# Kernel optimization log

Hardware: AMD Instinct MI355X
Metric: run time of the kernel (lower is better)

## Reference

```python
import jax, jax.numpy as jnp
import numpy as np

D_MODEL = 1024
N_HEADS = 16
CHUNK = 64
EPS = 1e-6


def elu_plus_1(x):
    return jax.nn.elu(x) + 1.0


def setup_inputs() -> dict:
    key = jax.random.key(0)
    kx, kq, kk, kv, ko = jax.random.split(key, 5)
    B, T = 4, 4096
    # xavier_uniform for square (D, D) weights: limit = sqrt(6/(D+D))
    lim = float(np.sqrt(6.0 / (D_MODEL + D_MODEL)))
    mk = lambda k: jax.random.uniform(k, (D_MODEL, D_MODEL), jnp.float32, -lim, lim)
    return {
        "x": jax.random.normal(kx, (B, T, D_MODEL), jnp.float32),
        "W_q": mk(kq),
        "W_k": mk(kk),
        "W_v": mk(kv),
        "W_o": mk(ko),
    }


def reference(x, W_q, W_k, W_v, W_o):
    B, T, D = x.shape
    H = N_HEADS
    dk = D // H
    dv = dk
    C = CHUNK
    N = T // C  # T chosen divisible by chunk size (no padding needed)

    q = (x @ W_q.T).reshape(B, T, H, dk)
    k = (x @ W_k.T).reshape(B, T, H, dk)
    v = (x @ W_v.T).reshape(B, T, H, dv)

    phi_q = elu_plus_1(q).reshape(B, N, C, H, dk)
    phi_k = elu_plus_1(k).reshape(B, N, C, H, dk)
    vc = v.reshape(B, N, C, H, dv)

    # Per-chunk key-value outer products and key sums, then exclusive prefix
    # sums over chunks give the carried state S and normalizer z at each
    # chunk's start (same math as the sequential chunk loop).
    KV = jnp.einsum('bnchk,bnchv->bnhkv', phi_k, vc)      # (B,N,H,dk,dv)
    Ksum = phi_k.sum(axis=2)                               # (B,N,C->sum,H,dk) -> (B,N,H,dk)
    KV_cum = jnp.cumsum(KV, axis=1)
    Ksum_cum = jnp.cumsum(Ksum, axis=1)
    S_prefix = jnp.concatenate([jnp.zeros_like(KV_cum[:, :1]), KV_cum[:, :-1]], axis=1)
    z_prefix = jnp.concatenate([jnp.zeros_like(Ksum_cum[:, :1]), Ksum_cum[:, :-1]], axis=1)

    # Inter-chunk contribution from carried state
    inter = jnp.einsum('bnchk,bnhkv->bnchv', phi_q, S_prefix)   # (B,N,C,H,dv)
    z_inter = jnp.einsum('bnchk,bnhk->bnch', phi_q, z_prefix)   # (B,N,C,H)

    # Intra-chunk causal attention
    mask = jnp.tril(jnp.ones((C, C), dtype=x.dtype))
    attn = jnp.einsum('bnihk,bnjhk->bnhij', phi_q, phi_k) * mask  # (B,N,H,C,C)
    intra = jnp.einsum('bnhij,bnjhv->bnihv', attn, vc)            # (B,N,C,H,dv)
    z_intra = attn.sum(axis=-1).transpose(0, 1, 3, 2)             # (B,N,C,H)

    denom = jnp.clip((z_inter + z_intra)[..., None], 1e-6, None)
    y = (inter + intra) / denom                                   # (B,N,C,H,dv)
    y = y.reshape(B, T, H * dv)
    return y @ W_o.T
```

## Files before the change

kernel.cpp:

```cpp
#include <hip/hip_runtime.h>


typedef unsigned short u16;
typedef float  f32x4 __attribute__((ext_vector_type(4)));
typedef short  b16x8 __attribute__((ext_vector_type(8)));
typedef u16    u16x4 __attribute__((ext_vector_type(4)));
typedef u16    u16x8 __attribute__((ext_vector_type(8)));

#define DEVINL __device__ __forceinline__

DEVINL u16 f2b(float f) {
  unsigned u = __float_as_uint(f);
  return (u16)((u + 0x7fffu + ((u >> 16) & 1u)) >> 16);
}
DEVINL float b2f(u16 s) { return __uint_as_float(((unsigned)s) << 16); }

DEVINL f32x4 mfma16(b16x8 a, b16x8 b, f32x4 c) {
  return __builtin_amdgcn_mfma_f32_16x16x32_bf16(a, b, c, 0, 0, 0);
}

DEVINL float phi_elu1(float v) { return v > 0.f ? v + 1.f : __expf(v); }

__global__ void cvt_all(const float* __restrict__ x,
                        const float* __restrict__ Wq, const float* __restrict__ Wk,
                        const float* __restrict__ Wv, const float* __restrict__ Wo,
                        u16* __restrict__ xb, u16* __restrict__ wqb,
                        u16* __restrict__ wkb, u16* __restrict__ wvb,
                        u16* __restrict__ wob) {
  const float* in;
  u16* out;
  int blk0, nblk, n8;
  const int b = blockIdx.x;
  if (b < 2048) {
    in = x; out = xb; blk0 = b; nblk = 2048; n8 = 2097152;
  } else {
    const int w = (b - 2048) >> 7;
    blk0 = (b - 2048) & 127; nblk = 128; n8 = 131072;
    switch (w) {
      case 0: in = Wq; out = wqb; break;
      case 1: in = Wk; out = wkb; break;
      case 2: in = Wv; out = wvb; break;
      default: in = Wo; out = wob; break;
    }
  }
  const int stride = nblk * 256;
  for (int i = blk0 * 256 + threadIdx.x; i < n8; i += stride) {
    const float* p = in + (size_t)i * 8;
    f32x4 a = *(const f32x4*)p;
    f32x4 c = *(const f32x4*)(p + 4);
    u16x8 o;
    o[0] = f2b(a[0]); o[1] = f2b(a[1]); o[2] = f2b(a[2]); o[3] = f2b(a[3]);
    o[4] = f2b(c[0]); o[5] = f2b(c[1]); o[6] = f2b(c[2]); o[7] = f2b(c[3]);
    *(u16x8*)(out + (size_t)i * 8) = o;
  }
}

#define BAR_SB()                                                                \
  do {                                                                          \
    __builtin_amdgcn_s_barrier();                                               \
    __builtin_amdgcn_sched_barrier(0);                                          \
  } while (0)

#define GLOAD(s_, d_)                                                           \
  __builtin_amdgcn_global_load_lds(                                             \
      (const __attribute__((address_space(1))) void*)(s_),                      \
      (__attribute__((address_space(3))) void*)(d_), 16, 0, 0)

template <bool PHI, typename OT>
__global__ __launch_bounds__(512, 2) void gemm256g(const u16* __restrict__ A,
                                                   const u16* __restrict__ B,
                                                   OT* __restrict__ C, int M, int N) {
  __shared__ char lds[131072];
  const int tid = threadIdx.x, wid = tid >> 6, l = tid & 63;
  const int l15 = l & 15, lg = l >> 4;
  const int wr = wid >> 2, wc = wid & 3;
  const int ntn = N >> 8;
  const int nwg = gridDim.x, bid = blockIdx.x;
  const int cpx = nwg >> 3;
  const int sb = (bid & 7) * cpx + (bid >> 3);
  const int tm = sb / ntn, tn = sb - tm * ntn;
  const int colX0 = (lg * 16) ^ ((l15 & 7) << 4);
  const int colX1 = (64 + lg * 16) ^ ((l15 & 7) << 4);
  char* ldsA = lds + wr * 16384 + l15 * 128;
  char* ldsB = lds + 32768 + (wc >> 1) * 16384 + ((wc & 1) * 64 + l15) * 128;
  const int srow = tid >> 3;
  const int scol = ((((tid & 7) * 16) ^ ((srow & 7) << 4)) >> 1);
  const u16* sA = A + (size_t)(tm * 256 + srow) * 1024 + scol;
  const u16* sB = B + (size_t)(tn * 256 + srow) * 1024 + scol;
  char* ldsStage = lds + wid * 1024;

#define STAGE(tt, h)                                                            \
  do {                                                                          \
    const u16* s_ = ((h) < 2 ? sA : sB) + (size_t)(((h) & 1) * 128) * 1024 +    \
                    (size_t)(tt) * 64;                                          \
    char* d_ = ldsStage + (((tt) & 1) << 16) + ((h) < 2 ? 0 : 32768) +          \
               (((h) & 1) << 14);                                               \
    GLOAD(s_, d_);                                                              \
    GLOAD(s_ + 64 * 1024, d_ + 8192);                                           \
  } while (0)

  f32x4 acc[8][4];
#pragma unroll
  for (int i = 0; i < 8; i++)
#pragma unroll
    for (int j = 0; j < 4; j++) acc[i][j] = f32x4{0.f, 0.f, 0.f, 0.f};

  STAGE(0, 0); STAGE(0, 1); STAGE(0, 2); STAGE(0, 3);
  STAGE(1, 2); STAGE(1, 3);
  asm volatile("s_waitcnt vmcnt(4)" ::: "memory");

  b16x8 a0[4], a1[4], b0[4], b1[4];
  for (int t = 0; t < 16; ++t) {
    const int cb = (t & 1) << 16;
    BAR_SB();
#pragma unroll
    for (int fm = 0; fm < 4; fm++) {
      a0[fm] = *(const b16x8*)(ldsA + cb + fm * 2048 + colX0);
      a1[fm] = *(const b16x8*)(ldsA + cb + (4 + fm) * 2048 + colX0);
    }
#pragma unroll
    for (int fn = 0; fn < 4; fn++) b0[fn] = *(const b16x8*)(ldsB + cb + fn * 2048 + colX0);
    if (t < 15) { STAGE(t + 1, 0); STAGE(t + 1, 1); }
    __builtin_amdgcn_s_setprio(1);
#pragma unroll
    for (int fm = 0; fm < 4; fm++)
#pragma unroll
      for (int fn = 0; fn < 4; fn++) {
        acc[fm][fn] = mfma16(a0[fm], b0[fn], acc[fm][fn]);
        acc[4 + fm][fn] = mfma16(a1[fm], b0[fn], acc[4 + fm][fn]);
      }
    __builtin_amdgcn_s_setprio(0);
    BAR_SB();
#pragma unroll
    for (int fm = 0; fm < 4; fm++) {
      a0[fm] = *(const b16x8*)(ldsA + cb + fm * 2048 + colX1);
      a1[fm] = *(const b16x8*)(ldsA + cb + (4 + fm) * 2048 + colX1);
    }
#pragma unroll
    for (int fn = 0; fn < 4; fn++) b1[fn] = *(const b16x8*)(ldsB + cb + fn * 2048 + colX1);
    if (t < 14) { STAGE(t + 2, 2); STAGE(t + 2, 3); }
    __builtin_amdgcn_s_setprio(1);
#pragma unroll
    for (int fm = 0; fm < 4; fm++)
#pragma unroll
      for (int fn = 0; fn < 4; fn++) {
        acc[fm][fn] = mfma16(a0[fm], b1[fn], acc[fm][fn]);
        acc[4 + fm][fn] = mfma16(a1[fm], b1[fn], acc[4 + fm][fn]);
      }
    __builtin_amdgcn_s_setprio(0);
    if (t < 14) asm volatile("s_waitcnt vmcnt(4)" ::: "memory");
    else        asm volatile("s_waitcnt vmcnt(0)" ::: "memory");
  }
#undef STAGE

#pragma unroll
  for (int fm = 0; fm < 8; ++fm)
#pragma unroll
    for (int fn = 0; fn < 4; ++fn)
#pragma unroll
      for (int r = 0; r < 4; ++r) {
        size_t grow = (size_t)tm * 256 + wr * 128 + fm * 16 + lg * 4 + r;
        size_t gcol = (size_t)tn * 256 + wc * 64 + fn * 16 + l15;
        float v = acc[fm][fn][r];
        if (PHI) v = phi_elu1(v);
        OT* p = C + grow * (size_t)N + gcol;
        if constexpr (sizeof(OT) == 2) *p = (OT)f2b(v);
        else                           *p = (OT)v;
      }
}

template <bool PHI, typename OT>
__global__ __launch_bounds__(256, 2) void gemm128(const u16* __restrict__ A,
                                                  const u16* __restrict__ B,
                                                  OT* __restrict__ C, int M, int N) {
  __shared__ char lds[65536];
  const int tid = threadIdx.x, wid = tid >> 6, l = tid & 63;
  const int l15 = l & 15, lg = l >> 4;
  const int wr = wid >> 1, wc = wid & 1;
  const int ntn = N >> 7;
  const int nwg = gridDim.x, bid = blockIdx.x;
  const int cpx = nwg >> 3;
  const int sb = (bid & 7) * cpx + (bid >> 3);
  const int tm = sb / ntn, tn = sb - tm * ntn;
  const int colX0 = (lg * 16) ^ ((l15 & 7) << 4);
  const int colX1 = (64 + lg * 16) ^ ((l15 & 7) << 4);
  char* ldsA = lds + (wr * 64 + l15) * 128;
  char* ldsB = lds + 16384 + (wc * 64 + l15) * 128;
  const int srow = tid >> 3;
  const int scol = ((((tid & 7) * 16) ^ ((srow & 7) << 4)) >> 1);
  const u16* sA = A + (size_t)(tm * 128 + srow) * 1024 + scol;
  const u16* sB = B + (size_t)(tn * 128 + srow) * 1024 + scol;
  char* ldsStage = lds + wid * 1024;

#define STAGE(tt, h)                                                            \
  do {                                                                          \
    const u16* s_ = ((h) < 2 ? sA : sB) + (size_t)(((h) & 1) * 64) * 1024 +     \
                    (size_t)(tt) * 64;                                          \
    char* d_ = ldsStage + (((tt) & 1) << 15) + ((h) < 2 ? 0 : 16384) +          \
               (((h) & 1) << 13);                                               \
    GLOAD(s_, d_);                                                              \
    GLOAD(s_ + 32 * 1024, d_ + 4096);                                           \
  } while (0)

  f32x4 acc[4][4];
#pragma unroll
  for (int i = 0; i < 4; i++)
#pragma unroll
    for (int j = 0; j < 4; j++) acc[i][j] = f32x4{0.f, 0.f, 0.f, 0.f};

  STAGE(0, 0); STAGE(0, 1); STAGE(0, 2); STAGE(0, 3);
  STAGE(1, 2); STAGE(1, 3);
  asm volatile("s_waitcnt vmcnt(4)" ::: "memory");

  b16x8 af[4], bf[4];
  for (int t = 0; t < 16; ++t) {
    const int cb = (t & 1) << 15;
    BAR_SB();
#pragma unroll
    for (int fm = 0; fm < 4; fm++) af[fm] = *(const b16x8*)(ldsA + cb + fm * 2048 + colX0);
#pragma unroll
    for (int fn = 0; fn < 4; fn++) bf[fn] = *(const b16x8*)(ldsB + cb + fn * 2048 + colX0);
    if (t < 15) { STAGE(t + 1, 0); STAGE(t + 1, 1); }
    __builtin_amdgcn_s_setprio(1);
#pragma unroll
    for (int fm = 0; fm < 4; fm++)
#pragma unroll
      for (int fn = 0; fn < 4; fn++) acc[fm][fn] = mfma16(af[fm], bf[fn], acc[fm][fn]);
    __builtin_amdgcn_s_setprio(0);
    BAR_SB();
#pragma unroll
    for (int fm = 0; fm < 4; fm++) af[fm] = *(const b16x8*)(ldsA + cb + fm * 2048 + colX1);
#pragma unroll
    for (int fn = 0; fn < 4; fn++) bf[fn] = *(const b16x8*)(ldsB + cb + fn * 2048 + colX1);
    if (t < 14) { STAGE(t + 2, 2); STAGE(t + 2, 3); }
    __builtin_amdgcn_s_setprio(1);
#pragma unroll
    for (int fm = 0; fm < 4; fm++)
#pragma unroll
      for (int fn = 0; fn < 4; fn++) acc[fm][fn] = mfma16(af[fm], bf[fn], acc[fm][fn]);
    __builtin_amdgcn_s_setprio(0);
    if (t < 14) asm volatile("s_waitcnt vmcnt(4)" ::: "memory");
    else        asm volatile("s_waitcnt vmcnt(0)" ::: "memory");
  }
#undef STAGE

#pragma unroll
  for (int fm = 0; fm < 4; ++fm)
#pragma unroll
    for (int fn = 0; fn < 4; ++fn)
#pragma unroll
      for (int r = 0; r < 4; ++r) {
        size_t grow = (size_t)tm * 128 + wr * 64 + fm * 16 + lg * 4 + r;
        size_t gcol = (size_t)tn * 128 + wc * 64 + fn * 16 + l15;
        float v = acc[fm][fn][r];
        if (PHI) v = phi_elu1(v);
        OT* p = C + grow * (size_t)N + gcol;
        if constexpr (sizeof(OT) == 2) *p = (OT)f2b(v);
        else                           *p = (OT)v;
      }
}

__global__ __launch_bounds__(256, 2) void kv_kernel(const u16* __restrict__ phiK,
                                                    const u16* __restrict__ vT,
                                                    u16* __restrict__ KVT,
                                                    float* __restrict__ Ksum) {
  __shared__ u16 tile[4][64][68];
  const int tid = threadIdx.x, wid = tid >> 6, l = tid & 63, l15 = l & 15, lg = l >> 4;
  const int bid = blockIdx.x, hg = bid & 3, bn = bid >> 2, n = bn & 63, b = bn >> 6;
  const int h = hg * 4 + wid;
  const size_t row0 = (size_t)b * 4096 + n * 64;
  const int dcol = h * 64;
  const size_t cb = (size_t)b * 4096 + n * 64 + lg * 8;

  b16x8 af[4][2];
#pragma unroll
  for (int fm = 0; fm < 4; fm++)
#pragma unroll
    for (int ks = 0; ks < 2; ks++)
      af[fm][ks] = *(const b16x8*)(vT + (size_t)(h * 64 + fm * 16 + l15) * 16384 + cb + ks * 32);

  u16 (*tw)[68] = tile[wid];
#pragma unroll
  for (int i = 0; i < 8; i++) {
    int tok = i * 8 + (l >> 3);
    int c8 = (l & 7) * 8;
    u16x8 v = *(const u16x8*)(phiK + (row0 + tok) * 1024 + dcol + c8);
    *(u16x4*)(&tw[tok][c8]) = u16x4{v[0], v[1], v[2], v[3]};
    *(u16x4*)(&tw[tok][c8 + 4]) = u16x4{v[4], v[5], v[6], v[7]};
  }
  __syncthreads();

  b16x8 bf[4][2];
#pragma unroll
  for (int fn = 0; fn < 4; fn++)
#pragma unroll
    for (int ks = 0; ks < 2; ks++) {
      b16x8 t;
#pragma unroll
      for (int j = 0; j < 8; j++)
        t[j] = (short)tw[lg * 8 + ks * 32 + j][fn * 16 + l15];
      bf[fn][ks] = t;
    }

  f32x4 acc[4][4];
#pragma unroll
  for (int i = 0; i < 4; i++)
#pragma unroll
    for (int j = 0; j < 4; j++) acc[i][j] = f32x4{0.f, 0.f, 0.f, 0.f};
#pragma unroll
  for (int ks = 0; ks < 2; ks++)
#pragma unroll
    for (int fm = 0; fm < 4; fm++)
#pragma unroll
      for (int fn = 0; fn < 4; fn++) acc[fm][fn] = mfma16(af[fm][ks], bf[fn][ks], acc[fm][fn]);

  float ksum[4] = {0.f, 0.f, 0.f, 0.f};
#pragma unroll
  for (int fn = 0; fn < 4; fn++) {
#pragma unroll
    for (int ks = 0; ks < 2; ks++)
#pragma unroll
      for (int j = 0; j < 8; j++) ksum[fn] += b2f((u16)bf[fn][ks][j]);
    ksum[fn] += __shfl_xor(ksum[fn], 16);
    ksum[fn] += __shfl_xor(ksum[fn], 32);
  }
  const size_t ob = (size_t)(b * 16 + h) * 64 + n;
  if (l < 16) {
#pragma unroll
    for (int fn = 0; fn < 4; fn++) Ksum[ob * 64 + fn * 16 + l15] = ksum[fn];
  }
#pragma unroll
  for (int fm = 0; fm < 4; fm++)
#pragma unroll
    for (int fn = 0; fn < 4; fn++)
#pragma unroll
      for (int r = 0; r < 4; r++)
        KVT[ob * 4096 + (size_t)(fm * 16 + lg * 4 + r) * 64 + fn * 16 + l15] =
            f2b(acc[fm][fn][r]);
}

__global__ __launch_bounds__(256) void scan_s(const u16* __restrict__ KVT,
                                              u16* __restrict__ ST,
                                              const float* __restrict__ Ksum,
                                              float* __restrict__ zpre) {
  if (blockIdx.x >= 512) {
    const int gi = (blockIdx.x - 512) * 256 + threadIdx.x;
    const size_t bh = gi >> 6;
    const int dk = gi & 63;
    float acc = 0.f;
    for (int n = 0; n < 64; n++) {
      size_t idx = (bh * 64 + n) * 64 + dk;
      zpre[idx] = acc;
      acc += Ksum[idx];
    }
    return;
  }
  const size_t base2 = (size_t)(blockIdx.x >> 3) * 64 * 2048 +
                       (blockIdx.x & 7) * 256 + threadIdx.x;
  const unsigned* KV32 = (const unsigned*)KVT;
  unsigned* ST32 = (unsigned*)ST;
  float ac0 = 0.f, ac1 = 0.f;
  unsigned v[4], w[4];
#pragma unroll
  for (int i = 0; i < 4; i++) v[i] = KV32[base2 + (size_t)i * 2048];
  for (int n = 0; n < 64; n += 4) {
    if (n < 60) {
#pragma unroll
      for (int i = 0; i < 4; i++) w[i] = KV32[base2 + (size_t)(n + 4 + i) * 2048];
    } else {
#pragma unroll
      for (int i = 0; i < 4; i++) w[i] = 0u;
    }
#pragma unroll
    for (int i = 0; i < 4; i++) {
      ST32[base2 + (size_t)(n + i) * 2048] =
          (unsigned)f2b(ac0) | ((unsigned)f2b(ac1) << 16);
      ac0 += b2f((u16)(v[i] & 0xffff));
      ac1 += b2f((u16)(v[i] >> 16));
    }
#pragma unroll
    for (int i = 0; i < 4; i++) v[i] = w[i];
  }
}

__global__ __launch_bounds__(256, 2) void attn_out(const u16* __restrict__ phiQ,
                                                   const u16* __restrict__ phiK,
                                                   const u16* __restrict__ vT,
                                                   const u16* __restrict__ ST,
                                                   const float* __restrict__ zpre,
                                                   u16* __restrict__ Y) {
  __shared__ char lds[4 * 8192 + 4 * 256];
  const int tid = threadIdx.x, wid = tid >> 6, l = tid & 63, l15 = l & 15, lg = l >> 4;
  const int bid = blockIdx.x, hg = bid & 3, bn = bid >> 2, n = bn & 63, b = bn >> 6;
  const int h = hg * 4 + wid;
  const size_t row0 = (size_t)b * 4096 + n * 64;
  const int dcol = h * 64;

  b16x8 qf[4][2];
#pragma unroll
  for (int fi = 0; fi < 4; fi++)
#pragma unroll
    for (int ks = 0; ks < 2; ks++)
      qf[fi][ks] = *(const b16x8*)(phiQ + (row0 + fi * 16 + l15) * 1024 + dcol + lg * 8 + ks * 32);

  f32x4 accT[4][4];
#pragma unroll
  for (int i = 0; i < 4; i++)
#pragma unroll
    for (int j = 0; j < 4; j++) accT[i][j] = f32x4{0.f, 0.f, 0.f, 0.f};
  {
    b16x8 kf[4][2];
#pragma unroll
    for (int fj = 0; fj < 4; fj++)
#pragma unroll
      for (int ks = 0; ks < 2; ks++)
        kf[fj][ks] = *(const b16x8*)(phiK + (row0 + fj * 16 + l15) * 1024 + dcol + lg * 8 + ks * 32);
#pragma unroll
    for (int ks = 0; ks < 2; ks++)
#pragma unroll
      for (int fj = 0; fj < 4; fj++)
#pragma unroll
        for (int fi = 0; fi < 4; fi++)
          accT[fj][fi] = mfma16(kf[fj][ks], qf[fi][ks], accT[fj][fi]);
  }

  const size_t zb = ((size_t)(b * 16 + h) * 64 + n) * 64;
  float zi[4] = {0.f, 0.f, 0.f, 0.f};
#pragma unroll
  for (int ks = 0; ks < 2; ks++) {
    f32x4 z0 = *(const f32x4*)(zpre + zb + lg * 8 + ks * 32);
    f32x4 z1 = *(const f32x4*)(zpre + zb + lg * 8 + ks * 32 + 4);
#pragma unroll
    for (int fi = 0; fi < 4; fi++)
#pragma unroll
      for (int j = 0; j < 4; j++) {
        zi[fi] += b2f((u16)qf[fi][ks][j])     * z0[j];
        zi[fi] += b2f((u16)qf[fi][ks][j + 4]) * z1[j];
      }
  }

  char* abuf = lds + wid * 8192;
  float zt[4] = {0.f, 0.f, 0.f, 0.f};
#pragma unroll
  for (int fi = 0; fi < 4; fi++) {
    const int i = fi * 16 + l15;
    const int swz = (i & 7) << 4;
#pragma unroll
    for (int fj = 0; fj < 4; fj++) {
      f32x4 v = accT[fj][fi];
#pragma unroll
      for (int r = 0; r < 4; r++) {
        int j = fj * 16 + lg * 4 + r;
        if (j > i) v[r] = 0.f;
        zt[fi] += v[r];
      }
      unsigned w0 = (unsigned)f2b(v[0]) | ((unsigned)f2b(v[1]) << 16);
      unsigned w1 = (unsigned)f2b(v[2]) | ((unsigned)f2b(v[3]) << 16);
      int jb = (fj * 16 + lg * 4) * 2;
      *(unsigned*)(abuf + i * 128 + (jb ^ swz)) = w0;
      *(unsigned*)(abuf + i * 128 + ((jb + 4) ^ swz)) = w1;
    }
  }

  float* dbuf = (float*)(lds + 32768 + wid * 256);
#pragma unroll
  for (int fi = 0; fi < 4; fi++) {
    float z = zi[fi] + zt[fi];
    z += __shfl_xor(z, 16);
    z += __shfl_xor(z, 32);
    float rd = 1.f / fmaxf(z, 1e-6f);
    if (l < 16) dbuf[fi * 16 + l15] = rd;
  }
  __syncthreads();

  b16x8 stf[4][2], vf[4][2];
  const size_t stb = ((size_t)(b * 16 + h) * 64 + n) * 4096;
#pragma unroll
  for (int fn = 0; fn < 4; fn++)
#pragma unroll
    for (int ks = 0; ks < 2; ks++) {
      stf[fn][ks] = *(const b16x8*)(ST + stb + (size_t)(fn * 16 + l15) * 64 + lg * 8 + ks * 32);
      vf[fn][ks]  = *(const b16x8*)(vT + (size_t)(dcol + fn * 16 + l15) * 16384 +
                                    (size_t)b * 4096 + n * 64 + lg * 8 + ks * 32);
    }
  f32x4 acc[4][4];
#pragma unroll
  for (int i = 0; i < 4; i++)
#pragma unroll
    for (int j = 0; j < 4; j++) acc[i][j] = f32x4{0.f, 0.f, 0.f, 0.f};
#pragma unroll
  for (int ks = 0; ks < 2; ks++)
#pragma unroll
    for (int fm = 0; fm < 4; fm++)
#pragma unroll
      for (int fn = 0; fn < 4; fn++) acc[fm][fn] = mfma16(qf[fm][ks], stf[fn][ks], acc[fm][fn]);
#pragma unroll
  for (int fm = 0; fm < 4; fm++) {
    const int i = fm * 16 + l15;
    const int swz = (i & 7) << 4;
#pragma unroll
    for (int ks = 0; ks < 2; ks++) {
      b16x8 af = *(const b16x8*)(abuf + i * 128 + ((ks * 64 + lg * 16) ^ swz));
#pragma unroll
      for (int fn = 0; fn < 4; fn++) acc[fm][fn] = mfma16(af, vf[fn][ks], acc[fm][fn]);
    }
  }

#pragma unroll
  for (int fm = 0; fm < 4; fm++)
#pragma unroll
    for (int r = 0; r < 4; r++) {
      float rd = dbuf[fm * 16 + lg * 4 + r];
#pragma unroll
      for (int fn = 0; fn < 4; fn++)
        Y[(row0 + fm * 16 + lg * 4 + r) * 1024 + dcol + fn * 16 + l15] =
            f2b(acc[fm][fn][r] * rd);
    }
}

extern "C" void kernel_launch(void* const* d_in, const int* in_sizes, int n_in,
                              void* d_out, int out_size, void* d_ws, size_t ws_size,
                              hipStream_t stream) {
  const float* x  = (const float*)d_in[0];
  const float* Wq = (const float*)d_in[1];
  const float* Wk = (const float*)d_in[2];
  const float* Wv = (const float*)d_in[3];
  const float* Wo = (const float*)d_in[4];
  float* out = (float*)d_out;

  char* ws = (char*)d_ws;
  size_t off = 0;
  auto alloc = [&](size_t bytes) -> char* {
    char* p = ws + off;
    off += (bytes + 255) & ~(size_t)255;
    return p;
  };
  u16*   xb   = (u16*)alloc(33554432);
  u16*   wqb  = (u16*)alloc(2097152);
  u16*   wkb  = (u16*)alloc(2097152);
  u16*   wvb  = (u16*)alloc(2097152);
  u16*   wob  = (u16*)alloc(2097152);
  u16*   phiQ = (u16*)alloc(33554432);
  u16*   phiK = (u16*)alloc(33554432);
  u16*   vT   = (u16*)alloc(33554432);
  u16*   KVT  = (u16*)alloc(33554432);
  float* Ksum = (float*)alloc(1048576);
  u16*   ST   = (u16*)alloc(33554432);
  float* zpre = (float*)alloc(1048576);
  u16*   y    = xb;

  cvt_all<<<2560, 256, 0, stream>>>(x, Wq, Wk, Wv, Wo, xb, wqb, wkb, wvb, wob);

  gemm128<true, u16><<<1024, 256, 0, stream>>>(xb, wqb, phiQ, 16384, 1024);
  gemm256g<true, u16><<<256, 512, 0, stream>>>(xb, wkb, phiK, 16384, 1024);
  gemm256g<false, u16><<<256, 512, 0, stream>>>(wvb, xb, vT, 1024, 16384);

  kv_kernel<<<1024, 256, 0, stream>>>(phiK, vT, KVT, Ksum);
  scan_s<<<528, 256, 0, stream>>>(KVT, ST, Ksum, zpre);
  attn_out<<<1024, 256, 0, stream>>>(phiQ, phiK, vT, ST, zpre, y);

  gemm256g<false, float><<<256, 512, 0, stream>>>(y, wob, out, 16384, 1024);
}
```

Measured before the change: 229.5 us.

## Replace Q-projection 128-tile GEMM with 256-tile GEMM loading B directly to registers

The Q projection GEMM changes from 128x128 tiles with 4 waves to 256x256 tiles with 8 waves. Only the A operand is staged through LDS. Each wave loads its B fragments straight from global memory into registers, double-buffered across K halves, with one barrier per K step instead of two. This is meant to raise data reuse and cut LDS traffic and synchronisation, at the cost of more registers and uncoalesced direct global loads for B.

```diff
diff --git a/kernel.cpp b/kernel.cpp
--- a/kernel.cpp
+++ b/kernel.cpp
@@ -170,88 +170,110 @@
 }
 
 template <bool PHI, typename OT>
-__global__ __launch_bounds__(256, 2) void gemm128(const u16* __restrict__ A,
-                                                  const u16* __restrict__ B,
-                                                  OT* __restrict__ C, int M, int N) {
+__global__ __launch_bounds__(512, 2) void gemm256d(const u16* __restrict__ A,
+                                                   const u16* __restrict__ B,
+                                                   OT* __restrict__ C, int M, int N) {
   __shared__ char lds[65536];
   const int tid = threadIdx.x, wid = tid >> 6, l = tid & 63;
   const int l15 = l & 15, lg = l >> 4;
-  const int wr = wid >> 1, wc = wid & 1;
-  const int ntn = N >> 7;
+  const int wr = wid >> 2, wc = wid & 3;
+  const int ntn = N >> 8;
   const int nwg = gridDim.x, bid = blockIdx.x;
   const int cpx = nwg >> 3;
   const int sb = (bid & 7) * cpx + (bid >> 3);
   const int tm = sb / ntn, tn = sb - tm * ntn;
   const int colX0 = (lg * 16) ^ ((l15 & 7) << 4);
   const int colX1 = (64 + lg * 16) ^ ((l15 & 7) << 4);
-  char* ldsA = lds + (wr * 64 + l15) * 128;
-  char* ldsB = lds + 16384 + (wc * 64 + l15) * 128;
+  char* ldsA = lds + wr * 16384 + l15 * 128;
   const int srow = tid >> 3;
   const int scol = ((((tid & 7) * 16) ^ ((srow & 7) << 4)) >> 1);
-  const u16* sA = A + (size_t)(tm * 128 + srow) * 1024 + scol;
-  const u16* sB = B + (size_t)(tn * 128 + srow) * 1024 + scol;
+  const u16* sA = A + (size_t)(tm * 256 + srow) * 1024 + scol;
   char* ldsStage = lds + wid * 1024;
-
-#define STAGE(tt, h)                                                            \
+  const u16* bp[4];
+#pragma unroll
+  for (int fn = 0; fn < 4; fn++)
+    bp[fn] = B + (size_t)(tn * 256 + wc * 64 + fn * 16 + l15) * 1024 + lg * 8;
+
+#define STAGEA(tt)                                                              \
   do {                                                                          \
-    const u16* s_ = ((h) < 2 ? sA : sB) + (size_t)(((h) & 1) * 64) * 1024 +     \
-                    (size_t)(tt) * 64;                                          \
-    char* d_ = ldsStage + (((tt) & 1) << 15) + ((h) < 2 ? 0 : 16384) +          \
-               (((h) & 1) << 13);                                               \
+    const u16* s_ = sA + (size_t)(tt) * 64;                                     \
+    char* d_ = ldsStage + (((tt) & 1) << 15);                                   \
     GLOAD(s_, d_);                                                              \
-    GLOAD(s_ + 32 * 1024, d_ + 4096);                                           \
+    GLOAD(s_ + 65536, d_ + 8192);                                               \
+    GLOAD(s_ + 131072, d_ + 16384);                                             \
+    GLOAD(s_ + 196608, d_ + 24576);                                             \
   } while (0)
 
-  f32x4 acc[4][4];
-#pragma unroll
-  for (int i = 0; i < 4; i++)
+  f32x4 acc[8][4];
+#pragma unroll
+  for (int i = 0; i < 8; i++)
 #pragma unroll
     for (int j = 0; j < 4; j++) acc[i][j] = f32x4{0.f, 0.f, 0.f, 0.f};
 
-  STAGE(0, 0); STAGE(0, 1); STAGE(0, 2); STAGE(0, 3);
-  STAGE(1, 2); STAGE(1, 3);
-  asm volatile("s_waitcnt vmcnt(4)" ::: "memory");
-
-  b16x8 af[4], bf[4];
+  b16x8 bk0[4], bk1[4];
+  STAGEA(0);
+#pragma unroll
+  for (int fn = 0; fn < 4; fn++) bk0[fn] = *(const b16x8*)(bp[fn]);
+#pragma unroll
+  for (int fn = 0; fn < 4; fn++) bk1[fn] = *(const b16x8*)(bp[fn] + 32);
+  asm volatile("s_waitcnt vmcnt(8)" ::: "memory");
+  BAR_SB();
+
+  b16x8 a0[4], a1[4];
   for (int t = 0; t < 16; ++t) {
     const int cb = (t & 1) << 15;
+#pragma unroll
+    for (int fm = 0; fm < 4; fm++) {
+      a0[fm] = *(const b16x8*)(ldsA + cb + fm * 2048 + colX0);
+      a1[fm] = *(const b16x8*)(ldsA + cb + (4 + fm) * 2048 + colX0);
+    }
+    if (t < 15) STAGEA(t + 1);
+    __builtin_amdgcn_s_setprio(1);
+#pragma unroll
+    for (int fm = 0; fm < 4; fm++)
+#pragma unroll
+      for (int fn = 0; fn < 4; fn++) {
+        acc[fm][fn] = mfma16(a0[fm], bk0[fn], acc[fm][fn]);
+        acc[4 + fm][fn] = mfma16(a1[fm], bk0[fn], acc[4 + fm][fn]);
+      }
+    __builtin_amdgcn_s_setprio(0);
+    if (t < 15) {
+#pragma unroll
+      for (int fn = 0; fn < 4; fn++) bk0[fn] = *(const b16x8*)(bp[fn] + (t + 1) * 64);
+    }
+#pragma unroll
+    for (int fm = 0; fm < 4; fm++) {
+      a0[fm] = *(const b16x8*)(ldsA + cb + fm * 2048 + colX1);
+      a1[fm] = *(const b16x8*)(ldsA + cb + (4 + fm) * 2048 + colX1);
+    }
+    __builtin_amdgcn_s_setprio(1);
+#pragma unroll
+    for (int fm = 0; fm < 4; fm++)
+#pragma unroll
+      for (int fn = 0; fn < 4; fn++) {
+        acc[fm][fn] = mfma16(a0[fm], bk1[fn], acc[fm][fn]);
+        acc[4 + fm][fn] = mfma16(a1[fm], bk1[fn], acc[4 + fm][fn]);
+      }
+    __builtin_amdgcn_s_setprio(0);
+    if (t < 15) {
+#pragma unroll
+      for (int fn = 0; fn < 4; fn++) bk1[fn] = *(const b16x8*)(bp[fn] + (t + 1) * 64 + 32);
+      asm volatile("s_waitcnt vmcnt(8)" ::: "memory");
+    } else {
+      asm volatile("s_waitcnt vmcnt(0)" ::: "memory");
+    }
     BAR_SB();
-#pragma unroll
-    for (int fm = 0; fm < 4; fm++) af[fm] = *(const b16x8*)(ldsA + cb + fm * 2048 + colX0);
-#pragma unroll
-    for (int fn = 0; fn < 4; fn++) bf[fn] = *(const b16x8*)(ldsB + cb + fn * 2048 + colX0);
-    if (t < 15) { STAGE(t + 1, 0); STAGE(t + 1, 1); }
-    __builtin_amdgcn_s_setprio(1);
-#pragma unroll
-    for (int fm = 0; fm < 4; fm++)
-#pragma unroll
-      for (int fn = 0; fn < 4; fn++) acc[fm][fn] = mfma16(af[fm], bf[fn], acc[fm][fn]);
-    __builtin_amdgcn_s_setprio(0);
-    BAR_SB();
-#pragma unroll
-    for (int fm = 0; fm < 4; fm++) af[fm] = *(const b16x8*)(ldsA + cb + fm * 2048 + colX1);
-#pragma unroll
-    for (int fn = 0; fn < 4; fn++) bf[fn] = *(const b16x8*)(ldsB + cb + fn * 2048 + colX1);
-    if (t < 14) { STAGE(t + 2, 2); STAGE(t + 2, 3); }
-    __builtin_amdgcn_s_setprio(1);
-#pragma unroll
-    for (int fm = 0; fm < 4; fm++)
-#pragma unroll
-      for (int fn = 0; fn < 4; fn++) acc[fm][fn] = mfma16(af[fm], bf[fn], acc[fm][fn]);
-    __builtin_amdgcn_s_setprio(0);
-    if (t < 14) asm volatile("s_waitcnt vmcnt(4)" ::: "memory");
-    else        asm volatile("s_waitcnt vmcnt(0)" ::: "memory");
-  }
-#undef STAGE
-
-#pragma unroll
-  for (int fm = 0; fm < 4; ++fm)
+  }
+#undef STAGEA
+
+#pragma unroll
+  for (int fm = 0; fm < 8; ++fm)
 #pragma unroll
     for (int fn = 0; fn < 4; ++fn)
 #pragma unroll
       for (int r = 0; r < 4; ++r) {
-        size_t grow = (size_t)tm * 128 + wr * 64 + fm * 16 + lg * 4 + r;
-        size_t gcol = (size_t)tn * 128 + wc * 64 + fn * 16 + l15;
+        size_t grow = (size_t)tm * 256 + wr * 128 + fm * 16 + lg * 4 + r;
+        size_t gcol = (size_t)tn * 256 + wc * 64 + fn * 16 + l15;
         float v = acc[fm][fn][r];
         if (PHI) v = phi_elu1(v);
         OT* p = C + grow * (size_t)N + gcol;
@@ -551,7 +573,7 @@
 
   cvt_all<<<2560, 256, 0, stream>>>(x, Wq, Wk, Wv, Wo, xb, wqb, wkb, wvb, wob);
 
-  gemm128<true, u16><<<1024, 256, 0, stream>>>(xb, wqb, phiQ, 16384, 1024);
+  gemm256d<true, u16><<<256, 512, 0, stream>>>(xb, wqb, phiQ, 16384, 1024);
   gemm256g<true, u16><<<256, 512, 0, stream>>>(xb, wkb, phiK, 16384, 1024);
   gemm256g<false, u16><<<256, 512, 0, stream>>>(wvb, xb, vT, 1024, 16384);
 
```

Result: slower. 244.2 us (+6.4%).

## Replace 128-tile Q projection GEMM with 256-tile K32 double-buffered kernel

Applied to the files above, without the earlier changes.

The Q projection GEMM moves from a 128x128 tile kernel with 4 waves to a new 256x256 tile kernel with 8 waves. It uses K-steps of 32, a 64-byte LDS row layout with an XOR swizzle, double buffering, and a full vmcnt(0) wait plus barrier each iteration. The larger tile raises operand reuse and cuts the grid from 1024 to 256 workgroups, which means fewer global and LDS loads per FLOP. In exchange it uses more registers (launch bounds of 4 blocks per CU may cause register pressure or spills), leaves less overlap between loads and MFMA, and makes the epilogue a shared macro.

```diff
diff --git a/kernel.cpp b/kernel.cpp
--- a/kernel.cpp
+++ b/kernel.cpp
@@ -65,6 +65,19 @@
   __builtin_amdgcn_global_load_lds(                                             \
       (const __attribute__((address_space(1))) void*)(s_),                      \
       (__attribute__((address_space(3))) void*)(d_), 16, 0, 0)
+
+#define GEMM_EPILOGUE                                                           \
+  _Pragma("unroll") for (int fm = 0; fm < 8; ++fm)                              \
+    _Pragma("unroll") for (int fn = 0; fn < 4; ++fn)                            \
+      _Pragma("unroll") for (int r = 0; r < 4; ++r) {                           \
+        size_t grow = (size_t)tm * 256 + wr * 128 + fm * 16 + lg * 4 + r;       \
+        size_t gcol = (size_t)tn * 256 + wc * 64 + fn * 16 + l15;               \
+        float v = acc[fm][fn][r];                                               \
+        if (PHI) v = phi_elu1(v);                                               \
+        OT* p = C + grow * (size_t)N + gcol;                                    \
+        if constexpr (sizeof(OT) == 2) *p = (OT)f2b(v);                         \
+        else                           *p = (OT)v;                              \
+      }
 
 template <bool PHI, typename OT>
 __global__ __launch_bounds__(512, 2) void gemm256g(const u16* __restrict__ A,
@@ -153,111 +166,70 @@
   }
 #undef STAGE
 
-#pragma unroll
-  for (int fm = 0; fm < 8; ++fm)
-#pragma unroll
-    for (int fn = 0; fn < 4; ++fn)
-#pragma unroll
-      for (int r = 0; r < 4; ++r) {
-        size_t grow = (size_t)tm * 256 + wr * 128 + fm * 16 + lg * 4 + r;
-        size_t gcol = (size_t)tn * 256 + wc * 64 + fn * 16 + l15;
-        float v = acc[fm][fn][r];
-        if (PHI) v = phi_elu1(v);
-        OT* p = C + grow * (size_t)N + gcol;
-        if constexpr (sizeof(OT) == 2) *p = (OT)f2b(v);
-        else                           *p = (OT)v;
-      }
+  GEMM_EPILOGUE
 }
 
 template <bool PHI, typename OT>
-__global__ __launch_bounds__(256, 2) void gemm128(const u16* __restrict__ A,
-                                                  const u16* __restrict__ B,
-                                                  OT* __restrict__ C, int M, int N) {
+__global__ __launch_bounds__(512, 4) void gemm256k(const u16* __restrict__ A,
+                                                   const u16* __restrict__ B,
+                                                   OT* __restrict__ C, int M, int N) {
   __shared__ char lds[65536];
   const int tid = threadIdx.x, wid = tid >> 6, l = tid & 63;
   const int l15 = l & 15, lg = l >> 4;
-  const int wr = wid >> 1, wc = wid & 1;
-  const int ntn = N >> 7;
+  const int wr = wid >> 2, wc = wid & 3;
+  const int ntn = N >> 8;
   const int nwg = gridDim.x, bid = blockIdx.x;
   const int cpx = nwg >> 3;
   const int sb = (bid & 7) * cpx + (bid >> 3);
   const int tm = sb / ntn, tn = sb - tm * ntn;
-  const int colX0 = (lg * 16) ^ ((l15 & 7) << 4);
-  const int colX1 = (64 + lg * 16) ^ ((l15 & 7) << 4);
-  char* ldsA = lds + (wr * 64 + l15) * 128;
-  char* ldsB = lds + 16384 + (wc * 64 + l15) * 128;
-  const int srow = tid >> 3;
-  const int scol = ((((tid & 7) * 16) ^ ((srow & 7) << 4)) >> 1);
-  const u16* sA = A + (size_t)(tm * 128 + srow) * 1024 + scol;
-  const u16* sB = B + (size_t)(tn * 128 + srow) * 1024 + scol;
+  const int colX = (lg * 16) ^ (((l15 >> 1) & 3) << 4);
+  char* ldsA = lds + (wr * 128 + l15) * 64 + colX;
+  char* ldsB = lds + 16384 + (wc * 64 + l15) * 64 + colX;
+  const int srow = tid >> 2;
+  const int scol = ((((tid & 3) * 16) ^ (((tid >> 3) & 3) << 4)) >> 1);
+  const u16* sA = A + (size_t)(tm * 256 + srow) * 1024 + scol;
+  const u16* sB = B + (size_t)(tn * 256 + srow) * 1024 + scol;
   char* ldsStage = lds + wid * 1024;
 
-#define STAGE(tt, h)                                                            \
+#define STAGEK(tt)                                                              \
   do {                                                                          \
-    const u16* s_ = ((h) < 2 ? sA : sB) + (size_t)(((h) & 1) * 64) * 1024 +     \
-                    (size_t)(tt) * 64;                                          \
-    char* d_ = ldsStage + (((tt) & 1) << 15) + ((h) < 2 ? 0 : 16384) +          \
-               (((h) & 1) << 13);                                               \
-    GLOAD(s_, d_);                                                              \
-    GLOAD(s_ + 32 * 1024, d_ + 4096);                                           \
+    const int bb = ((tt) & 1) << 15;                                            \
+    GLOAD(sA + (size_t)(tt) * 32, ldsStage + bb);                               \
+    GLOAD(sA + 131072 + (size_t)(tt) * 32, ldsStage + bb + 8192);               \
+    GLOAD(sB + (size_t)(tt) * 32, ldsStage + bb + 16384);                       \
+    GLOAD(sB + 131072 + (size_t)(tt) * 32, ldsStage + bb + 24576);              \
   } while (0)
 
-  f32x4 acc[4][4];
-#pragma unroll
-  for (int i = 0; i < 4; i++)
+  f32x4 acc[8][4];
+#pragma unroll
+  for (int i = 0; i < 8; i++)
 #pragma unroll
     for (int j = 0; j < 4; j++) acc[i][j] = f32x4{0.f, 0.f, 0.f, 0.f};
 
-  STAGE(0, 0); STAGE(0, 1); STAGE(0, 2); STAGE(0, 3);
-  STAGE(1, 2); STAGE(1, 3);
-  asm volatile("s_waitcnt vmcnt(4)" ::: "memory");
-
-  b16x8 af[4], bf[4];
-  for (int t = 0; t < 16; ++t) {
+  STAGEK(0);
+  asm volatile("s_waitcnt vmcnt(0)" ::: "memory");
+  BAR_SB();
+
+  b16x8 af[8], bf[4];
+  for (int t = 0; t < 32; ++t) {
     const int cb = (t & 1) << 15;
-    BAR_SB();
-#pragma unroll
-    for (int fm = 0; fm < 4; fm++) af[fm] = *(const b16x8*)(ldsA + cb + fm * 2048 + colX0);
-#pragma unroll
-    for (int fn = 0; fn < 4; fn++) bf[fn] = *(const b16x8*)(ldsB + cb + fn * 2048 + colX0);
-    if (t < 15) { STAGE(t + 1, 0); STAGE(t + 1, 1); }
+#pragma unroll
+    for (int fm = 0; fm < 8; fm++) af[fm] = *(const b16x8*)(ldsA + cb + fm * 1024);
+#pragma unroll
+    for (int fn = 0; fn < 4; fn++) bf[fn] = *(const b16x8*)(ldsB + cb + fn * 1024);
+    if (t < 31) STAGEK(t + 1);
     __builtin_amdgcn_s_setprio(1);
 #pragma unroll
-    for (int fm = 0; fm < 4; fm++)
+    for (int fm = 0; fm < 8; fm++)
 #pragma unroll
       for (int fn = 0; fn < 4; fn++) acc[fm][fn] = mfma16(af[fm], bf[fn], acc[fm][fn]);
     __builtin_amdgcn_s_setprio(0);
+    asm volatile("s_waitcnt vmcnt(0)" ::: "memory");
     BAR_SB();
-#pragma unroll
-    for (int fm = 0; fm < 4; fm++) af[fm] = *(const b16x8*)(ldsA + cb + fm * 2048 + colX1);
-#pragma unroll
-    for (int fn = 0; fn < 4; fn++) bf[fn] = *(const b16x8*)(ldsB + cb + fn * 2048 + colX1);
-    if (t < 14) { STAGE(t + 2, 2); STAGE(t + 2, 3); }
-    __builtin_amdgcn_s_setprio(1);
-#pragma unroll
-    for (int fm = 0; fm < 4; fm++)
-#pragma unroll
-      for (int fn = 0; fn < 4; fn++) acc[fm][fn] = mfma16(af[fm], bf[fn], acc[fm][fn]);
-    __builtin_amdgcn_s_setprio(0);
-    if (t < 14) asm volatile("s_waitcnt vmcnt(4)" ::: "memory");
-    else        asm volatile("s_waitcnt vmcnt(0)" ::: "memory");
-  }
-#undef STAGE
-
-#pragma unroll
-  for (int fm = 0; fm < 4; ++fm)
-#pragma unroll
-    for (int fn = 0; fn < 4; ++fn)
-#pragma unroll
-      for (int r = 0; r < 4; ++r) {
-        size_t grow = (size_t)tm * 128 + wr * 64 + fm * 16 + lg * 4 + r;
-        size_t gcol = (size_t)tn * 128 + wc * 64 + fn * 16 + l15;
-        float v = acc[fm][fn][r];
-        if (PHI) v = phi_elu1(v);
-        OT* p = C + grow * (size_t)N + gcol;
-        if constexpr (sizeof(OT) == 2) *p = (OT)f2b(v);
-        else                           *p = (OT)v;
-      }
+  }
+#undef STAGEK
+
+  GEMM_EPILOGUE
 }
 
 __global__ __launch_bounds__(256, 2) void kv_kernel(const u16* __restrict__ phiK,
@@ -551,7 +523,7 @@
 
   cvt_all<<<2560, 256, 0, stream>>>(x, Wq, Wk, Wv, Wo, xb, wqb, wkb, wvb, wob);
 
-  gemm128<true, u16><<<1024, 256, 0, stream>>>(xb, wqb, phiQ, 16384, 1024);
+  gemm256k<true, u16><<<256, 512, 0, stream>>>(xb, wqb, phiQ, 16384, 1024);
   gemm256g<true, u16><<<256, 512, 0, stream>>>(xb, wkb, phiK, 16384, 1024);
   gemm256g<false, u16><<<256, 512, 0, stream>>>(wvb, xb, vT, 1024, 16384);
 
```

Result: slower. 468.8 us (+104.3%).

## Shrink Q-projection GEMM K-tile to 32 for four blocks per CU

Applied to the files above, without the earlier changes.

Rewrites the 128x128 Q-projection GEMM to stage K-tiles of 32 instead of 64. This halves LDS to 32KB per block and raises launch bounds to allow 4 blocks per CU. The LDS swizzle and staging layout are reworked for 64-byte rows, and the loop now runs 32 iterations with a full vmcnt(0) wait and barrier each time. The aim is more occupancy to hide latency, at the cost of more barriers per unit of work and a shallower prefetch overlap.

```diff
diff --git a/kernel.cpp b/kernel.cpp
--- a/kernel.cpp
+++ b/kernel.cpp
@@ -170,10 +170,10 @@
 }
 
 template <bool PHI, typename OT>
-__global__ __launch_bounds__(256, 2) void gemm128(const u16* __restrict__ A,
-                                                  const u16* __restrict__ B,
-                                                  OT* __restrict__ C, int M, int N) {
-  __shared__ char lds[65536];
+__global__ __launch_bounds__(256, 4) void gemm128q(const u16* __restrict__ A,
+                                                   const u16* __restrict__ B,
+                                                   OT* __restrict__ C, int M, int N) {
+  __shared__ char lds[32768];
   const int tid = threadIdx.x, wid = tid >> 6, l = tid & 63;
   const int l15 = l & 15, lg = l >> 4;
   const int wr = wid >> 1, wc = wid & 1;
@@ -182,24 +182,22 @@
   const int cpx = nwg >> 3;
   const int sb = (bid & 7) * cpx + (bid >> 3);
   const int tm = sb / ntn, tn = sb - tm * ntn;
-  const int colX0 = (lg * 16) ^ ((l15 & 7) << 4);
-  const int colX1 = (64 + lg * 16) ^ ((l15 & 7) << 4);
-  char* ldsA = lds + (wr * 64 + l15) * 128;
-  char* ldsB = lds + 16384 + (wc * 64 + l15) * 128;
-  const int srow = tid >> 3;
-  const int scol = ((((tid & 7) * 16) ^ ((srow & 7) << 4)) >> 1);
+  const int colX = (lg * 16) ^ (((l15 >> 1) & 3) << 4);
+  char* ldsA = lds + (wr * 64 + l15) * 64 + colX;
+  char* ldsB = lds + 8192 + (wc * 64 + l15) * 64 + colX;
+  const int srow = tid >> 2;
+  const int scol = ((((tid & 3) * 16) ^ (((srow >> 1) & 3) << 4)) >> 1);
   const u16* sA = A + (size_t)(tm * 128 + srow) * 1024 + scol;
   const u16* sB = B + (size_t)(tn * 128 + srow) * 1024 + scol;
   char* ldsStage = lds + wid * 1024;
 
-#define STAGE(tt, h)                                                            \
+#define STAGEQ(tt)                                                              \
   do {                                                                          \
-    const u16* s_ = ((h) < 2 ? sA : sB) + (size_t)(((h) & 1) * 64) * 1024 +     \
-                    (size_t)(tt) * 64;                                          \
-    char* d_ = ldsStage + (((tt) & 1) << 15) + ((h) < 2 ? 0 : 16384) +          \
-               (((h) & 1) << 13);                                               \
-    GLOAD(s_, d_);                                                              \
-    GLOAD(s_ + 32 * 1024, d_ + 4096);                                           \
+    const int bb = ((tt) & 1) << 14;                                            \
+    GLOAD(sA + (size_t)(tt) * 32, ldsStage + bb);                               \
+    GLOAD(sA + 65536 + (size_t)(tt) * 32, ldsStage + bb + 4096);                \
+    GLOAD(sB + (size_t)(tt) * 32, ldsStage + bb + 8192);                        \
+    GLOAD(sB + 65536 + (size_t)(tt) * 32, ldsStage + bb + 12288);               \
   } while (0)
 
   f32x4 acc[4][4];
@@ -208,41 +206,28 @@
 #pragma unroll
     for (int j = 0; j < 4; j++) acc[i][j] = f32x4{0.f, 0.f, 0.f, 0.f};
 
-  STAGE(0, 0); STAGE(0, 1); STAGE(0, 2); STAGE(0, 3);
-  STAGE(1, 2); STAGE(1, 3);
-  asm volatile("s_waitcnt vmcnt(4)" ::: "memory");
+  STAGEQ(0);
+  asm volatile("s_waitcnt vmcnt(0)" ::: "memory");
+  BAR_SB();
 
   b16x8 af[4], bf[4];
-  for (int t = 0; t < 16; ++t) {
-    const int cb = (t & 1) << 15;
-    BAR_SB();
-#pragma unroll
-    for (int fm = 0; fm < 4; fm++) af[fm] = *(const b16x8*)(ldsA + cb + fm * 2048 + colX0);
-#pragma unroll
-    for (int fn = 0; fn < 4; fn++) bf[fn] = *(const b16x8*)(ldsB + cb + fn * 2048 + colX0);
-    if (t < 15) { STAGE(t + 1, 0); STAGE(t + 1, 1); }
+  for (int t = 0; t < 32; ++t) {
+    const int cb = (t & 1) << 14;
+#pragma unroll
+    for (int fm = 0; fm < 4; fm++) af[fm] = *(const b16x8*)(ldsA + cb + fm * 1024);
+#pragma unroll
+    for (int fn = 0; fn < 4; fn++) bf[fn] = *(const b16x8*)(ldsB + cb + fn * 1024);
+    if (t < 31) STAGEQ(t + 1);
     __builtin_amdgcn_s_setprio(1);
 #pragma unroll
     for (int fm = 0; fm < 4; fm++)
 #pragma unroll
       for (int fn = 0; fn < 4; fn++) acc[fm][fn] = mfma16(af[fm], bf[fn], acc[fm][fn]);
     __builtin_amdgcn_s_setprio(0);
+    asm volatile("s_waitcnt vmcnt(0)" ::: "memory");
     BAR_SB();
-#pragma unroll
-    for (int fm = 0; fm < 4; fm++) af[fm] = *(const b16x8*)(ldsA + cb + fm * 2048 + colX1);
-#pragma unroll
-    for (int fn = 0; fn < 4; fn++) bf[fn] = *(const b16x8*)(ldsB + cb + fn * 2048 + colX1);
-    if (t < 14) { STAGE(t + 2, 2); STAGE(t + 2, 3); }
-    __builtin_amdgcn_s_setprio(1);
-#pragma unroll
-    for (int fm = 0; fm < 4; fm++)
-#pragma unroll
-      for (int fn = 0; fn < 4; fn++) acc[fm][fn] = mfma16(af[fm], bf[fn], acc[fm][fn]);
-    __builtin_amdgcn_s_setprio(0);
-    if (t < 14) asm volatile("s_waitcnt vmcnt(4)" ::: "memory");
-    else        asm volatile("s_waitcnt vmcnt(0)" ::: "memory");
-  }
-#undef STAGE
+  }
+#undef STAGEQ
 
 #pragma unroll
   for (int fm = 0; fm < 4; ++fm)
@@ -551,7 +536,7 @@
 
   cvt_all<<<2560, 256, 0, stream>>>(x, Wq, Wk, Wv, Wo, xb, wqb, wkb, wvb, wob);
 
-  gemm128<true, u16><<<1024, 256, 0, stream>>>(xb, wqb, phiQ, 16384, 1024);
+  gemm128q<true, u16><<<1024, 256, 0, stream>>>(xb, wqb, phiQ, 16384, 1024);
   gemm256g<true, u16><<<256, 512, 0, stream>>>(xb, wkb, phiK, 16384, 1024);
   gemm256g<false, u16><<<256, 512, 0, stream>>>(wvb, xb, vT, 1024, 16384);
 
```

After: 237.4 us. 3.5% more time.
